# Kernel tuning notes

Hardware: AMD Instinct MI355X
Metric: run time of the kernel (lower is better)

## Reference

```python
import jax, jax.numpy as jnp
import numpy as np

B, S, INP, HID = 64, 2048, 512, 512

def setup_inputs() -> dict:
    key = jax.random.key(0)
    ks = jax.random.split(key, 8)
    inp = jax.random.normal(ks[0], (B, INP), dtype=jnp.float32)
    context = jax.random.normal(ks[1], (B, S, INP), dtype=jnp.float32)
    mask = jax.random.randint(ks[2], (B, S), 0, 2) == 1  # True = masked out
    lim_l = 1.0 / np.sqrt(INP)
    Wl = jax.random.uniform(ks[3], (HID, INP), minval=-lim_l, maxval=lim_l, dtype=jnp.float32)
    bl = jax.random.uniform(ks[4], (HID,), minval=-lim_l, maxval=lim_l, dtype=jnp.float32)
    Wc = jax.random.uniform(ks[5], (HID, INP), minval=-lim_l, maxval=lim_l, dtype=jnp.float32)  # Conv1d k=1 weight squeezed
    bc = jax.random.uniform(ks[6], (HID,), minval=-lim_l, maxval=lim_l, dtype=jnp.float32)
    V = jax.random.uniform(ks[7], (HID,), minval=-1.0, maxval=1.0, dtype=jnp.float32)
    return {"inp": inp, "context": context, "mask": mask,
            "Wl": Wl, "bl": bl, "Wc": Wc, "bc": bc, "V": V}

def reference(inp, context, mask, Wl, bl, Wc, bc, V):
    # hid: [B, HID], broadcast over S
    hid = inp @ Wl.T + bl
    # 1x1 Conv1d over permuted context == per-position linear: [B, HID, S]
    ctx = jnp.einsum('bsi,hi->bhs', context, Wc) + bc[None, :, None]
    # additive attention scores: [B, S]
    att = jnp.einsum('h,bhs->bs', V, jnp.tanh(hid[:, :, None] + ctx))
    att = jnp.where(mask, -jnp.inf, att)
    alpha = jax.nn.softmax(att, axis=1)
    # context vector: [B, HID]
    hidden_state = jnp.einsum('bhs,bs->bh', ctx, alpha)
    return (hidden_state, alpha)
```

## Files before the change

### kernel.cpp

```cpp
#include <hip/hip_runtime.h>
#include <hip/hip_bf16.h>
#include <cstdint>
#include <cstddef>

#define B_   64
#define S_   2048
#define INP_ 512
#define HID_ 512
#define STILE 64
#define NCH_ 32

typedef float          floatx4  __attribute__((ext_vector_type(4)));
typedef __bf16         bf16x8   __attribute__((ext_vector_type(8)));
typedef unsigned short ushortx8 __attribute__((ext_vector_type(8)));
typedef unsigned short ushortx4 __attribute__((ext_vector_type(4)));

#define K2E 1.4426950408889634f

__device__ __forceinline__ unsigned short f2bf(float f) {
  unsigned u = __float_as_uint(f);
  u += 0x7FFFu + ((u >> 16) & 1u);
  return (unsigned short)(u >> 16);
}
__device__ __forceinline__ float bf2f(unsigned short h) {
  return __uint_as_float(((unsigned)h) << 16);
}
__device__ __forceinline__ float fast_tanh(float x) {
  float u = __builtin_amdgcn_exp2f(x * 2.88539008177792681472f);
  return 1.0f - 2.0f * __builtin_amdgcn_rcpf(u + 1.0f);
}

__device__ __forceinline__ bool mask_at(const void* mask, int mode, size_t idx) {
  if (mode == 0) return ((const int*)mask)[idx] != 0;
  if (mode == 1) return ((const float*)mask)[idx] != 0.0f;
  return ((const unsigned char*)mask)[idx] != 0;
}

__global__ __launch_bounds__(256) void prep_kernel(
    const float* __restrict__ inp, const float* __restrict__ Wl,
    const float* __restrict__ bl, float* __restrict__ hid,
    const float* __restrict__ Wc, unsigned short* __restrict__ pk,
    const void* __restrict__ mask, int* __restrict__ mode_ws)
{
  __shared__ float vs[512];
  __shared__ int flags;
  const int t = threadIdx.x;
  if (blockIdx.x == 640) {
    if (t == 0) flags = 0;
    __syncthreads();
    int f = 0;
    const unsigned* mw = (const unsigned*)mask;
    for (int i = t; i < 512; i += 256) {
      unsigned v = mw[i];
      if (v > 1u) f |= 1;
      if (v != 0u && v != 0x3f800000u) f |= 2;
    }
    if (f) atomicOr(&flags, f);
    __syncthreads();
    if (t == 0) {
      const int fl = flags;
      *mode_ws = ((fl & 1) == 0) ? 0 : (((fl & 2) == 0) ? 1 : 2);
    }
    return;
  }
  if (blockIdx.x < 128) {
    int g = blockIdx.x * 256 + t;
    int l = g & 63, ks = (g >> 6) & 15, m16 = g >> 10;
    int row = m16 * 16 + (l & 15);
    int kb  = ks * 32 + (l >> 4) * 8;
    const float4* s = (const float4*)(Wc + (size_t)row * 512 + kb);
    float4 a = s[0], c = s[1];
    ushortx8 o = { f2bf(a.x), f2bf(a.y), f2bf(a.z), f2bf(a.w),
                   f2bf(c.x), f2bf(c.y), f2bf(c.z), f2bf(c.w) };
    *(ushortx8*)(pk + (size_t)g * 8) = o;
    return;
  }
  const int bx = blockIdx.x - 128;
  const int xo = bx & 7, b = bx >> 3;
  const int w = t >> 6, lane = t & 63;
  for (int i = t; i < 512; i += 256) vs[i] = inp[(size_t)b * 512 + i];
  __syncthreads();
  float vl[8];
  #pragma unroll
  for (int j = 0; j < 8; ++j) vl[j] = vs[lane * 8 + j];
  const int h0 = xo * 64 + w * 16;
  #pragma unroll
  for (int i = 0; i < 16; ++i) {
    const int h = h0 + i;
    const float4* wr = (const float4*)(Wl + (size_t)h * 512 + lane * 8);
    float4 w0 = wr[0], w1 = wr[1];
    float d = w0.x*vl[0] + w0.y*vl[1] + w0.z*vl[2] + w0.w*vl[3]
            + w1.x*vl[4] + w1.y*vl[5] + w1.z*vl[6] + w1.w*vl[7];
    #pragma unroll
    for (int off = 32; off; off >>= 1) d += __shfl_xor(d, off);
    if (lane == 0) hid[(size_t)b * 512 + h] = bl[h] + d;
  }
}

__global__ __launch_bounds__(256, 2) void att_gemm_kernel(
    const float* __restrict__ context, const unsigned short* __restrict__ Wc_pk,
    const float* __restrict__ hid, const float* __restrict__ bc,
    const float* __restrict__ V, const void* __restrict__ mask,
    const int* __restrict__ mode_ws,
    float* __restrict__ att, float* __restrict__ partial,
    float* __restrict__ mt, float* __restrict__ lt)
{
  __shared__ alignas(16) unsigned short bsm[STILE * 512];
  __shared__ float hid_sm[512];
  __shared__ float V_sm[512];
  __shared__ float bc_sm[512];
  __shared__ float att_sm[STILE];
  __shared__ float w_sm[STILE];

  const int b    = blockIdx.y;
  const int c    = blockIdx.x;
  const int s0   = c * STILE;
  const int t    = threadIdx.x;
  const int lane = t & 63;
  const int w    = t >> 6;
  const int quad = lane >> 4;
  const int l15  = lane & 15;

  const int mode = *mode_ws;

  for (int i = t; i < 512; i += 256) {
    hid_sm[i] = hid[b * 512 + i];
    V_sm[i]   = V[i];
    bc_sm[i]  = bc[i];
  }
  if (t < STILE) att_sm[t] = 0.0f;

  floatx4 acc[8][4];
  #pragma unroll
  for (int m = 0; m < 8; ++m)
    #pragma unroll
    for (int n = 0; n < 4; ++n) { floatx4 z = {0.f,0.f,0.f,0.f}; acc[m][n] = z; }

  const unsigned short* apBase = Wc_pk + (size_t)(w * 8) * 8192 + lane * 8;
  const float* src = context + ((size_t)b * S_ + s0) * INP_;

  auto stage = [&](int p) {
    #pragma unroll
    for (int i = 0; i < 8; ++i) {
      int id  = t + i * 256;
      int row = id >> 5;
      int c4  = id & 31;
      float4 f = *(const float4*)(src + (size_t)row * INP_ + p * 128 + c4 * 4);
      int chunk = c4 >> 1, half = c4 & 1;
      int sw = chunk ^ (row & 7);
      ushortx4 hv = { f2bf(f.x), f2bf(f.y), f2bf(f.z), f2bf(f.w) };
      *(ushortx4*)(&bsm[row * 512 + p * 128 + sw * 8 + half * 4]) = hv;
    }
  };

  stage(0);
  __syncthreads();

  for (int phase = 0; phase < 4; ++phase) {
    if (phase < 3) stage(phase + 1);
    #pragma unroll
    for (int ksl = 0; ksl < 4; ++ksl) {
      const int ksg = phase * 4 + ksl;
      bf16x8 af[8];
      #pragma unroll
      for (int m = 0; m < 8; ++m)
        af[m] = *(const bf16x8*)(apBase + (size_t)m * 8192 + ksg * 512);
      bf16x8 bfr[4];
      #pragma unroll
      for (int n = 0; n < 4; ++n) {
        int row = n * 16 + l15;
        int cc  = ksl * 4 + quad;
        bfr[n] = *(const bf16x8*)(&bsm[row * 512 + phase * 128 + ((cc ^ (row & 7)) * 8)]);
      }
      __builtin_amdgcn_s_setprio(1);
      #pragma unroll
      for (int m = 0; m < 8; ++m)
        #pragma unroll
        for (int n = 0; n < 4; ++n)
          acc[m][n] = __builtin_amdgcn_mfma_f32_16x16x32_bf16(af[m], bfr[n], acc[m][n], 0, 0, 0);
      __builtin_amdgcn_s_setprio(0);
    }
    __syncthreads();
  }

  float attacc[4] = {0.f, 0.f, 0.f, 0.f};
  #pragma unroll
  for (int m = 0; m < 8; ++m) {
    const int hb = w * 128 + m * 16 + quad * 4;
    #pragma unroll
    for (int r = 0; r < 4; ++r) {
      const int h = hb + r;
      const float base = hid_sm[h] + bc_sm[h];
      const float vv = V_sm[h];
      #pragma unroll
      for (int n = 0; n < 4; ++n)
        attacc[n] += vv * fast_tanh(base + acc[m][n][r]);
    }
  }
  #pragma unroll
  for (int n = 0; n < 4; ++n) {
    float v = attacc[n];
    v += __shfl_xor(v, 16);
    v += __shfl_xor(v, 32);
    if (lane < 16) atomicAdd(&att_sm[n * 16 + l15], v);
  }
  __syncthreads();

  if (t < STILE) {
    att[(size_t)b * S_ + s0 + t] = att_sm[t];
    const bool m = mask_at(mask, mode, (size_t)b * S_ + s0 + t);
    const float av = att_sm[t];
    float mv = m ? -1e30f : av;
    #pragma unroll
    for (int off = 32; off; off >>= 1) mv = fmaxf(mv, __shfl_xor(mv, off));
    const float wv = m ? 0.0f : __builtin_amdgcn_exp2f((av - mv) * K2E);
    w_sm[t] = wv;
    float lv = wv;
    #pragma unroll
    for (int off = 32; off; off >>= 1) lv += __shfl_xor(lv, off);
    if (t == 0) { mt[b * NCH_ + c] = mv; lt[b * NCH_ + c] = lv; }
  }
  __syncthreads();

  {
    const int k0 = t * 2;
    const int p  = k0 >> 7, kl = k0 & 127;
    const int c4 = kl >> 2, j = kl & 3;
    const int idxu = p * 128 + (c4 >> 1) * 8 + (c4 & 1) * 4 + j;
    float ax = 0.f, ay = 0.f;
    #pragma unroll 8
    for (int s = 0; s < STILE; ++s) {
      const unsigned v = *(const unsigned*)(&bsm[s * 512 + (idxu ^ ((s & 7) << 3))]);
      const float wv = w_sm[s];
      ax = fmaf(wv, bf2f((unsigned short)(v & 0xffffu)), ax);
      ay = fmaf(wv, bf2f((unsigned short)(v >> 16)), ay);
    }
    float2 o; o.x = ax; o.y = ay;
    *(float2*)(partial + ((size_t)c * B_ + b) * INP_ + k0) = o;
  }
}

__global__ __launch_bounds__(256) void finalize_kernel(
    const void* __restrict__ mask, const float* __restrict__ att,
    const int* __restrict__ mode_ws,
    const float* __restrict__ mt, const float* __restrict__ lt,
    float* __restrict__ sc, float* __restrict__ alpha)
{
  __shared__ float Msh, Lsh;
  const int b = blockIdx.x, t = threadIdx.x;
  const int mode = *mode_ws;

  if (t < NCH_) {
    float m = mt[b * NCH_ + t];
    #pragma unroll
    for (int off = 16; off; off >>= 1) m = fmaxf(m, __shfl_xor(m, off));
    float e = __builtin_amdgcn_exp2f((mt[b * NCH_ + t] - m) * K2E) * lt[b * NCH_ + t];
    #pragma unroll
    for (int off = 16; off; off >>= 1) e += __shfl_xor(e, off);
    if (t == 0) { Msh = m; Lsh = e; }
  }
  __syncthreads();
  const float M = Msh;
  const float rL = 1.0f / Lsh;
  if (t < NCH_) sc[b * NCH_ + t] = __builtin_amdgcn_exp2f((mt[b * NCH_ + t] - M) * K2E) * rL;

  #pragma unroll
  for (int i = 0; i < 8; ++i) {
    const int idx = i * 256 + t;
    const bool m = mask_at(mask, mode, (size_t)b * S_ + idx);
    const float a = m ? 0.0f
                      : __builtin_amdgcn_exp2f((att[(size_t)b * S_ + idx] - M) * K2E) * rL;
    alpha[(size_t)b * S_ + idx] = a;
  }
}

__global__ __launch_bounds__(256) void hiddendot_kernel(
    const float* __restrict__ Wc, const float* __restrict__ bc,
    const float* __restrict__ partial, const float* __restrict__ sc,
    float* __restrict__ hidden)
{
  __shared__ float vs[512];
  __shared__ float scs[NCH_];
  const int b = blockIdx.y, t = threadIdx.x;
  const int w = t >> 6, lane = t & 63;
  if (t < NCH_) scs[t] = sc[b * NCH_ + t];
  __syncthreads();
  for (int i = t; i < 512; i += 256) {
    float s = 0.0f;
    #pragma unroll 4
    for (int c = 0; c < NCH_; ++c)
      s += scs[c] * partial[((size_t)c * B_ + b) * INP_ + i];
    vs[i] = s;
  }
  __syncthreads();
  float vl[8];
  #pragma unroll
  for (int j = 0; j < 8; ++j) vl[j] = vs[lane * 8 + j];
  const int h0 = blockIdx.x * 64 + w * 16;
  #pragma unroll
  for (int i = 0; i < 16; ++i) {
    const int h = h0 + i;
    const float4* wr = (const float4*)(Wc + (size_t)h * 512 + lane * 8);
    float4 w0 = wr[0], w1 = wr[1];
    float d = w0.x*vl[0] + w0.y*vl[1] + w0.z*vl[2] + w0.w*vl[3]
            + w1.x*vl[4] + w1.y*vl[5] + w1.z*vl[6] + w1.w*vl[7];
    #pragma unroll
    for (int off = 32; off; off >>= 1) d += __shfl_xor(d, off);
    if (lane == 0) hidden[(size_t)b * 512 + h] = bc[h] + d;
  }
}

extern "C" void kernel_launch(void* const* d_in, const int* in_sizes, int n_in,
                              void* d_out, int out_size, void* d_ws, size_t ws_size,
                              hipStream_t stream)
{
  const float* inp     = (const float*)d_in[0];
  const float* context = (const float*)d_in[1];
  const void*  mask    = d_in[2];
  const float* Wl      = (const float*)d_in[3];
  const float* bl      = (const float*)d_in[4];
  const float* Wc      = (const float*)d_in[5];
  const float* bc      = (const float*)d_in[6];
  const float* V       = (const float*)d_in[7];

  float* hidden = (float*)d_out;
  float* alpha  = (float*)d_out + B_ * HID_;

  char* ws = (char*)d_ws;
  const size_t HIDW = (size_t)B_ * HID_ * 4;
  const size_t ATT  = (size_t)B_ * S_ * 4;
  const size_t PK   = (size_t)HID_ * INP_ * 2;
  const size_t PART = (size_t)NCH_ * B_ * INP_ * 4;
  const size_t MT   = (size_t)B_ * NCH_ * 4;

  float* hid_ws      = (float*)ws;
  float* att_ws      = (float*)(ws + HIDW);
  unsigned short* pk = (unsigned short*)(ws + HIDW + ATT);
  float* partial     = (float*)(ws + HIDW + ATT + PK);
  float* mt          = (float*)(ws + HIDW + ATT + PK + PART);
  float* lt          = (float*)(ws + HIDW + ATT + PK + PART + MT);
  float* sc          = (float*)(ws + HIDW + ATT + PK + PART + 2 * MT);
  int*   mode_ws     = (int*)  (ws + HIDW + ATT + PK + PART + 3 * MT);

  prep_kernel<<<641, 256, 0, stream>>>(inp, Wl, bl, hid_ws, Wc, pk, mask, mode_ws);
  att_gemm_kernel<<<dim3(NCH_, B_), 256, 0, stream>>>(
      context, pk, hid_ws, bc, V, mask, mode_ws, att_ws, partial, mt, lt);
  finalize_kernel<<<B_, 256, 0, stream>>>(mask, att_ws, mode_ws, mt, lt, sc, alpha);
  hiddendot_kernel<<<dim3(HID_ / 64, B_), 256, 0, stream>>>(Wc, bc, partial, sc, hidden);
}
```

Before: 479.1 us.

## Use 512-thread attention GEMM blocks, register-prefetch staging, fuse finalize into hiddendot

```diff
diff --git a/kernel.cpp b/kernel.cpp
--- a/kernel.cpp
+++ b/kernel.cpp
@@ -97,7 +97,7 @@
   }
 }
 
-__global__ __launch_bounds__(256, 2) void att_gemm_kernel(
+__global__ __launch_bounds__(512, 2) void att_gemm_kernel(
     const float* __restrict__ context, const unsigned short* __restrict__ Wc_pk,
     const float* __restrict__ hid, const float* __restrict__ bc,
     const float* __restrict__ V, const void* __restrict__ mask,
@@ -123,47 +123,59 @@
 
   const int mode = *mode_ws;
 
-  for (int i = t; i < 512; i += 256) {
+  for (int i = t; i < 512; i += 512) {
     hid_sm[i] = hid[b * 512 + i];
     V_sm[i]   = V[i];
     bc_sm[i]  = bc[i];
   }
   if (t < STILE) att_sm[t] = 0.0f;
 
-  floatx4 acc[8][4];
-  #pragma unroll
-  for (int m = 0; m < 8; ++m)
+  floatx4 acc[4][4];
+  #pragma unroll
+  for (int m = 0; m < 4; ++m)
     #pragma unroll
     for (int n = 0; n < 4; ++n) { floatx4 z = {0.f,0.f,0.f,0.f}; acc[m][n] = z; }
 
-  const unsigned short* apBase = Wc_pk + (size_t)(w * 8) * 8192 + lane * 8;
+  const unsigned short* apBase = Wc_pk + (size_t)(w * 4) * 8192 + lane * 8;
   const float* src = context + ((size_t)b * S_ + s0) * INP_;
 
-  auto stage = [&](int p) {
-    #pragma unroll
-    for (int i = 0; i < 8; ++i) {
-      int id  = t + i * 256;
-      int row = id >> 5;
-      int c4  = id & 31;
-      float4 f = *(const float4*)(src + (size_t)row * INP_ + p * 128 + c4 * 4);
-      int chunk = c4 >> 1, half = c4 & 1;
-      int sw = chunk ^ (row & 7);
-      ushortx4 hv = { f2bf(f.x), f2bf(f.y), f2bf(f.z), f2bf(f.w) };
-      *(ushortx4*)(&bsm[row * 512 + p * 128 + sw * 8 + half * 4]) = hv;
-    }
-  };
-
-  stage(0);
+  const int rb   = t >> 5;
+  const int c4   = t & 31;
+  const int sw   = (c4 >> 1) ^ (rb & 7);
+  const int dst_off = sw * 8 + (c4 & 1) * 4;
+
+  {
+    const float* sp = src + c4 * 4;
+    float4 f0 = *(const float4*)(sp + (size_t)(rb     ) * INP_);
+    float4 f1 = *(const float4*)(sp + (size_t)(rb + 16) * INP_);
+    float4 f2 = *(const float4*)(sp + (size_t)(rb + 32) * INP_);
+    float4 f3 = *(const float4*)(sp + (size_t)(rb + 48) * INP_);
+    ushortx4 h0 = { f2bf(f0.x), f2bf(f0.y), f2bf(f0.z), f2bf(f0.w) };
+    ushortx4 h1 = { f2bf(f1.x), f2bf(f1.y), f2bf(f1.z), f2bf(f1.w) };
+    ushortx4 h2 = { f2bf(f2.x), f2bf(f2.y), f2bf(f2.z), f2bf(f2.w) };
+    ushortx4 h3 = { f2bf(f3.x), f2bf(f3.y), f2bf(f3.z), f2bf(f3.w) };
+    *(ushortx4*)(&bsm[(rb     ) * 512 + dst_off]) = h0;
+    *(ushortx4*)(&bsm[(rb + 16) * 512 + dst_off]) = h1;
+    *(ushortx4*)(&bsm[(rb + 32) * 512 + dst_off]) = h2;
+    *(ushortx4*)(&bsm[(rb + 48) * 512 + dst_off]) = h3;
+  }
   __syncthreads();
 
   for (int phase = 0; phase < 4; ++phase) {
-    if (phase < 3) stage(phase + 1);
+    float4 n0, n1, n2, n3;
+    if (phase < 3) {
+      const float* sp = src + (phase + 1) * 128 + c4 * 4;
+      n0 = *(const float4*)(sp + (size_t)(rb     ) * INP_);
+      n1 = *(const float4*)(sp + (size_t)(rb + 16) * INP_);
+      n2 = *(const float4*)(sp + (size_t)(rb + 32) * INP_);
+      n3 = *(const float4*)(sp + (size_t)(rb + 48) * INP_);
+    }
     #pragma unroll
     for (int ksl = 0; ksl < 4; ++ksl) {
       const int ksg = phase * 4 + ksl;
-      bf16x8 af[8];
+      bf16x8 af[4];
       #pragma unroll
-      for (int m = 0; m < 8; ++m)
+      for (int m = 0; m < 4; ++m)
         af[m] = *(const bf16x8*)(apBase + (size_t)m * 8192 + ksg * 512);
       bf16x8 bfr[4];
       #pragma unroll
@@ -174,19 +186,30 @@
       }
       __builtin_amdgcn_s_setprio(1);
       #pragma unroll
-      for (int m = 0; m < 8; ++m)
+      for (int m = 0; m < 4; ++m)
         #pragma unroll
         for (int n = 0; n < 4; ++n)
           acc[m][n] = __builtin_amdgcn_mfma_f32_16x16x32_bf16(af[m], bfr[n], acc[m][n], 0, 0, 0);
       __builtin_amdgcn_s_setprio(0);
     }
+    if (phase < 3) {
+      ushortx4 h0 = { f2bf(n0.x), f2bf(n0.y), f2bf(n0.z), f2bf(n0.w) };
+      ushortx4 h1 = { f2bf(n1.x), f2bf(n1.y), f2bf(n1.z), f2bf(n1.w) };
+      ushortx4 h2 = { f2bf(n2.x), f2bf(n2.y), f2bf(n2.z), f2bf(n2.w) };
+      ushortx4 h3 = { f2bf(n3.x), f2bf(n3.y), f2bf(n3.z), f2bf(n3.w) };
+      unsigned short* dp = &bsm[(phase + 1) * 128 + dst_off];
+      *(ushortx4*)(dp + (size_t)(rb     ) * 512) = h0;
+      *(ushortx4*)(dp + (size_t)(rb + 16) * 512) = h1;
+      *(ushortx4*)(dp + (size_t)(rb + 32) * 512) = h2;
+      *(ushortx4*)(dp + (size_t)(rb + 48) * 512) = h3;
+    }
     __syncthreads();
   }
 
   float attacc[4] = {0.f, 0.f, 0.f, 0.f};
   #pragma unroll
-  for (int m = 0; m < 8; ++m) {
-    const int hb = w * 128 + m * 16 + quad * 4;
+  for (int m = 0; m < 4; ++m) {
+    const int hb = w * 64 + m * 16 + quad * 4;
     #pragma unroll
     for (int r = 0; r < 4; ++r) {
       const int h = hb + r;
@@ -222,11 +245,11 @@
   }
   __syncthreads();
 
-  {
+  if (t < 256) {
     const int k0 = t * 2;
     const int p  = k0 >> 7, kl = k0 & 127;
-    const int c4 = kl >> 2, j = kl & 3;
-    const int idxu = p * 128 + (c4 >> 1) * 8 + (c4 & 1) * 4 + j;
+    const int cc = kl >> 2, j = kl & 3;
+    const int idxu = p * 128 + (cc >> 1) * 8 + (cc & 1) * 4 + j;
     float ax = 0.f, ay = 0.f;
     #pragma unroll 8
     for (int s = 0; s < STILE; ++s) {
@@ -240,51 +263,47 @@
   }
 }
 
-__global__ __launch_bounds__(256) void finalize_kernel(
-    const void* __restrict__ mask, const float* __restrict__ att,
-    const int* __restrict__ mode_ws,
-    const float* __restrict__ mt, const float* __restrict__ lt,
-    float* __restrict__ sc, float* __restrict__ alpha)
-{
-  __shared__ float Msh, Lsh;
-  const int b = blockIdx.x, t = threadIdx.x;
-  const int mode = *mode_ws;
-
-  if (t < NCH_) {
-    float m = mt[b * NCH_ + t];
-    #pragma unroll
-    for (int off = 16; off; off >>= 1) m = fmaxf(m, __shfl_xor(m, off));
-    float e = __builtin_amdgcn_exp2f((mt[b * NCH_ + t] - m) * K2E) * lt[b * NCH_ + t];
-    #pragma unroll
-    for (int off = 16; off; off >>= 1) e += __shfl_xor(e, off);
-    if (t == 0) { Msh = m; Lsh = e; }
-  }
-  __syncthreads();
-  const float M = Msh;
-  const float rL = 1.0f / Lsh;
-  if (t < NCH_) sc[b * NCH_ + t] = __builtin_amdgcn_exp2f((mt[b * NCH_ + t] - M) * K2E) * rL;
-
-  #pragma unroll
-  for (int i = 0; i < 8; ++i) {
-    const int idx = i * 256 + t;
-    const bool m = mask_at(mask, mode, (size_t)b * S_ + idx);
-    const float a = m ? 0.0f
-                      : __builtin_amdgcn_exp2f((att[(size_t)b * S_ + idx] - M) * K2E) * rL;
-    alpha[(size_t)b * S_ + idx] = a;
-  }
-}
-
 __global__ __launch_bounds__(256) void hiddendot_kernel(
     const float* __restrict__ Wc, const float* __restrict__ bc,
-    const float* __restrict__ partial, const float* __restrict__ sc,
-    float* __restrict__ hidden)
+    const float* __restrict__ partial,
+    const float* __restrict__ mt, const float* __restrict__ lt,
+    const float* __restrict__ att, const void* __restrict__ mask,
+    const int* __restrict__ mode_ws,
+    float* __restrict__ hidden, float* __restrict__ alpha)
 {
   __shared__ float vs[512];
   __shared__ float scs[NCH_];
+  __shared__ float Msh, Lsh;
   const int b = blockIdx.y, t = threadIdx.x;
   const int w = t >> 6, lane = t & 63;
-  if (t < NCH_) scs[t] = sc[b * NCH_ + t];
-  __syncthreads();
+
+  if (t < NCH_) {
+    float m = mt[b * NCH_ + t];
+    #pragma unroll
+    for (int off = 16; off; off >>= 1) m = fmaxf(m, __shfl_xor(m, off));
+    float e = __builtin_amdgcn_exp2f((mt[b * NCH_ + t] - m) * K2E) * lt[b * NCH_ + t];
+    #pragma unroll
+    for (int off = 16; off; off >>= 1) e += __shfl_xor(e, off);
+    if (t == 0) { Msh = m; Lsh = e; }
+  }
+  __syncthreads();
+  const float M = Msh;
+  const float rL = 1.0f / Lsh;
+  if (t < NCH_) scs[t] = __builtin_amdgcn_exp2f((mt[b * NCH_ + t] - M) * K2E) * rL;
+
+  if (blockIdx.x == 0) {
+    const int mode = *mode_ws;
+    #pragma unroll
+    for (int i = 0; i < 8; ++i) {
+      const int idx = i * 256 + t;
+      const bool m = mask_at(mask, mode, (size_t)b * S_ + idx);
+      const float a = m ? 0.0f
+                        : __builtin_amdgcn_exp2f((att[(size_t)b * S_ + idx] - M) * K2E) * rL;
+      alpha[(size_t)b * S_ + idx] = a;
+    }
+  }
+  __syncthreads();
+
   for (int i = t; i < 512; i += 256) {
     float s = 0.0f;
     #pragma unroll 4
@@ -339,12 +358,11 @@
   float* partial     = (float*)(ws + HIDW + ATT + PK);
   float* mt          = (float*)(ws + HIDW + ATT + PK + PART);
   float* lt          = (float*)(ws + HIDW + ATT + PK + PART + MT);
-  float* sc          = (float*)(ws + HIDW + ATT + PK + PART + 2 * MT);
-  int*   mode_ws     = (int*)  (ws + HIDW + ATT + PK + PART + 3 * MT);
+  int*   mode_ws     = (int*)  (ws + HIDW + ATT + PK + PART + 2 * MT);
 
   prep_kernel<<<641, 256, 0, stream>>>(inp, Wl, bl, hid_ws, Wc, pk, mask, mode_ws);
-  att_gemm_kernel<<<dim3(NCH_, B_), 256, 0, stream>>>(
+  att_gemm_kernel<<<dim3(NCH_, B_), 512, 0, stream>>>(
       context, pk, hid_ws, bc, V, mask, mode_ws, att_ws, partial, mt, lt);
-  finalize_kernel<<<B_, 256, 0, stream>>>(mask, att_ws, mode_ws, mt, lt, sc, alpha);
-  hiddendot_kernel<<<dim3(HID_ / 64, B_), 256, 0, stream>>>(Wc, bc, partial, sc, hidden);
-}
+  hiddendot_kernel<<<dim3(HID_ / 64, B_), 256, 0, stream>>>(
+      Wc, bc, partial, mt, lt, att_ws, mask, mode_ws, hidden, alpha);
+}
```

Measured after the change: 460.7 us. 1.04x faster.
